# Performance work log

Hardware: AMD Instinct MI355X
Metric: run time of the kernel (lower is better)

## Reference

```python
import jax, jax.numpy as jnp
import numpy as np

NUM_USERS = 100000
NUM_ITEMS = 50000
N_NODES = NUM_USERS + NUM_ITEMS
N_INTERACTIONS = 1000000
LATENT_DIM = 32
K = 4
N_LAYERS = 3
BATCH = 4096


def setup_inputs() -> dict:
    key = jax.random.key(0)
    k_u, k_i = jax.random.split(key)
    # torch init: normal std=0.1
    user_emb = 0.1 * jax.random.normal(k_u, (NUM_USERS, LATENT_DIM * K), dtype=jnp.float32)
    item_emb = 0.1 * jax.random.normal(k_i, (NUM_ITEMS, LATENT_DIM * K), dtype=jnp.float32)
    # build symmetric normalized bipartite adjacency (LightGCN getSparseGraph)
    rng = np.random.default_rng(0)
    u = rng.integers(0, NUM_USERS, N_INTERACTIONS)
    it = rng.integers(0, NUM_ITEMS, N_INTERACTIONS)
    src = np.concatenate([u, it + NUM_USERS]).astype(np.int32)
    dst = np.concatenate([it + NUM_USERS, u]).astype(np.int32)
    deg = np.bincount(src, minlength=N_NODES).astype(np.float32)
    deg = np.maximum(deg, 1.0)
    val = (1.0 / np.sqrt(deg[src] * deg[dst])).astype(np.float32)
    users = rng.integers(0, NUM_USERS, BATCH).astype(np.int32)
    items = rng.integers(0, NUM_ITEMS, BATCH).astype(np.int32)
    return {
        "user_emb": user_emb,
        "item_emb": item_emb,
        "edge_src": jnp.asarray(src),
        "edge_dst": jnp.asarray(dst),
        "edge_val": jnp.asarray(val),
        "users": jnp.asarray(users),
        "items": jnp.asarray(items),
    }


def _computer(user_emb, item_emb, edge_src, edge_dst, edge_val):
    n_users = user_emb.shape[0]
    n = n_users + item_emb.shape[0]
    # [N, K, D] disentangled factor view of the K*D embedding
    x = jnp.concatenate([user_emb, item_emb], axis=0).reshape(n, K, -1)
    embs = [x]
    for _ in range(N_LAYERS):
        # SpMM over all K factor slices at once: out[dst] += val * x[src]
        msgs = x[edge_src] * edge_val[:, None, None]  # [E, K, D]
        x = jax.ops.segment_sum(msgs, edge_dst, num_segments=n)
        embs.append(x)
    light_out = jnp.mean(jnp.stack(embs, axis=1), axis=1)  # [N, K, D]
    return light_out[:n_users], light_out[n_users:]


def reference(user_emb, item_emb, edge_src, edge_dst, edge_val, users, items):
    all_users, all_items = _computer(user_emb, item_emb, edge_src, edge_dst, edge_val)
    u = all_users[users]   # [B, K, D]
    i = all_items[items]   # [B, K, D]
    return jnp.sum(u * i, axis=(-1, -2))  # [B]
```

## Files before the change

### kernel.cpp

```cpp
#include <hip/hip_runtime.h>

#define NUM_USERS 100000
#define NUM_ITEMS 50000
#define N_NODES   150000
#define N_EDGES   2000000
#define N_INTER   1000000
#define DIM       128
#define DIM4      32
#define BATCH     4096
#define B_SHIFT   9
#define BUCK_N    (1 << B_SHIFT)
#define NBUCK     ((N_NODES + BUCK_N - 1) >> B_SHIFT)
#define PAIRS     4096
#define NPBLK     ((N_INTER + PAIRS - 1) / PAIRS)
#define CAP       12288
#define CAPB      16384
#define MARK_BLOCKS 512
#define CONV_BLOCKS (((N_NODES + 1) * 8 + 255) / 256)

#define G0 16.0f
#define INV_G1 (1.0f / 64.0f)
#define INV_G2 (1.0f / 256.0f)

typedef __attribute__((ext_vector_type(4))) float f32x4;
typedef __attribute__((ext_vector_type(2))) float f32x2;

__device__ inline f32x2 f8x2_lo(unsigned w) { return __builtin_amdgcn_cvt_pk_f32_fp8(w, 0); }
__device__ inline f32x2 f8x2_hi(unsigned w) { return __builtin_amdgcn_cvt_pk_f32_fp8(w, 1); }
__device__ inline unsigned enc_lo(float a, float b, unsigned old) {
    return __builtin_amdgcn_cvt_pk_fp8_f32(a, b, old, 0);
}
__device__ inline unsigned enc_hi(float a, float b, unsigned old) {
    return __builtin_amdgcn_cvt_pk_fp8_f32(a, b, old, 1);
}


__global__ void bucket_scatter_kernel(const int* __restrict__ src,
                                      int* __restrict__ bcur,
                                      int* __restrict__ tmp) {
    __shared__ int lhist[NBUCK];
    __shared__ int lcur[NBUCK];
    int t = threadIdx.x;
    int base = blockIdx.x * PAIRS;
    for (int i = t; i < NBUCK; i += 512) lhist[i] = 0;
    __syncthreads();
    for (int i = 0; i < PAIRS / 512; ++i) {
        int gp = base + i * 512 + t;
        if (gp < N_INTER) {
            int u = src[gp];
            int v = src[N_INTER + gp];
            atomicAdd(&lhist[v >> B_SHIFT], 1);
            atomicAdd(&lhist[u >> B_SHIFT], 1);
        }
    }
    __syncthreads();
    for (int i = t; i < NBUCK; i += 512) {
        int c = lhist[i];
        lcur[i] = c ? (i * CAPB + atomicAdd(&bcur[i], c)) : 0;
    }
    __syncthreads();
    for (int i = 0; i < PAIRS / 512; ++i) {
        int gp = base + i * 512 + t;
        if (gp < N_INTER) {
            int u = src[gp];
            int v = src[N_INTER + gp];
            int bv = v >> B_SHIFT;
            int bu = u >> B_SHIFT;
            int pos0 = atomicAdd(&lcur[bv], 1);
            if (pos0 < (bv + 1) * CAPB)
                tmp[pos0] = (u << B_SHIFT) | (v & (BUCK_N - 1));
            int pos1 = atomicAdd(&lcur[bu], 1);
            if (pos1 < (bu + 1) * CAPB)
                tmp[pos1] = (v << B_SHIFT) | (u & (BUCK_N - 1));
        }
    }
}


__global__ void place_kernel(const int* __restrict__ bcur,
                             const int* __restrict__ tmp,
                             int* __restrict__ row_start,
                             float* __restrict__ rinv,
                             float* __restrict__ sdeg,
                             int* __restrict__ csr_src) {
    __shared__ int lhist[BUCK_N];
    __shared__ int lofs[BUCK_N];
    __shared__ int ssc[512];
    __shared__ int outbuf[CAP];
    int b = blockIdx.x;
    int t = threadIdx.x;

    int c = 0;
    if (t < NBUCK) {
        c = bcur[t];
        if (c > CAPB) c = CAPB;
    }
    ssc[t] = c;
    __syncthreads();
    for (int off = 1; off < 512; off <<= 1) {
        int v = (t >= off) ? ssc[t - off] : 0;
        __syncthreads();
        ssc[t] += v;
        __syncthreads();
    }
    int beg = (b == 0) ? 0 : ssc[b - 1];
    int end = ssc[b];
    int cnt = end - beg;
    int tbase = b * CAPB;
    int n0 = b << B_SHIFT;
    int n1 = n0 + BUCK_N; if (n1 > N_NODES) n1 = N_NODES;
    if (b == NBUCK - 1 && t == 0) row_start[N_NODES] = end;

    lhist[t] = 0;
    __syncthreads();
    for (int e = t; e < cnt; e += 512)
        atomicAdd(&lhist[tmp[tbase + e] & (BUCK_N - 1)], 1);
    __syncthreads();

    int v = lhist[t];
    ssc[t] = v;
    __syncthreads();
    for (int off = 1; off < 512; off <<= 1) {
        int u = (t >= off) ? ssc[t - off] : 0;
        __syncthreads();
        ssc[t] += u;
        __syncthreads();
    }
    int excl = ssc[t] - v;
    lofs[t] = excl;
    int node = n0 + t;
    if (node < n1) {
        row_start[node] = beg + excl;
        float d = (float)(v > 1 ? v : 1);
        float rr = rsqrtf(d);
        rinv[node] = rr;
        sdeg[node] = d * rr;
    }
    __syncthreads();

    if (cnt <= CAP) {
        for (int e = t; e < cnt; e += 512) {
            int p = tmp[tbase + e];
            int pos = atomicAdd(&lofs[p & (BUCK_N - 1)], 1);
            outbuf[pos] = p >> B_SHIFT;
        }
        __syncthreads();
        for (int i = t; i < cnt; i += 512) csr_src[beg + i] = outbuf[i];
    } else {
        for (int e = t; e < cnt; e += 512) {
            int p = tmp[tbase + e];
            int pos = atomicAdd(&lofs[p & (BUCK_N - 1)], 1);
            csr_src[beg + pos] = p >> B_SHIFT;
        }
    }
}


__global__ void mark_conv_kernel(const f32x4* __restrict__ ue4,
                                 const f32x4* __restrict__ ie4,
                                 const float* __restrict__ rinv,
                                 uint4* __restrict__ e16f8,
                                 uint4* __restrict__ w1f8,
                                 uint4* __restrict__ w2f8,
                                 const int* __restrict__ users,
                                 const int* __restrict__ items,
                                 const int* __restrict__ row_start,
                                 const int* __restrict__ csr_src,
                                 int* __restrict__ mark) {
    int bid = blockIdx.x;
    if (bid < MARK_BLOCKS) {
        int g = threadIdx.x >> 4;
        int lane = threadIdx.x & 15;
        int b = bid * 16 + g;
        int node = (b < BATCH) ? users[b] : (NUM_USERS + items[b - BATCH]);
        if (lane == 0) mark[node] = 1;
        int beg = row_start[node], end = row_start[node + 1];
        for (int e = beg + lane; e < end; e += 16) mark[csr_src[e]] = 1;
        return;
    }
    int i = (bid - MARK_BLOCKS) * 256 + threadIdx.x;
    const int total = (N_NODES + 1) * 8;
    if (i >= total) return;
    int n = i >> 3;
    if (n >= N_NODES) {
        uint4 z = make_uint4(0u, 0u, 0u, 0u);
        e16f8[i] = z;
        w1f8[i] = z;
        w2f8[i] = z;
        return;
    }
    int j = i & 7;
    const f32x4* row = (n < NUM_USERS) ? ue4 + (size_t)n * DIM4
                                       : ie4 + (size_t)(n - NUM_USERS) * DIM4;
    float r = rinv[n] * G0;
    f32x4 c0 = __builtin_nontemporal_load(&row[4 * j]);
    f32x4 c1 = __builtin_nontemporal_load(&row[4 * j + 1]);
    f32x4 c2 = __builtin_nontemporal_load(&row[4 * j + 2]);
    f32x4 c3 = __builtin_nontemporal_load(&row[4 * j + 3]);
    uint4 o;
    o.x = enc_hi(r * c0.z, r * c0.w, enc_lo(r * c0.x, r * c0.y, 0u));
    o.y = enc_hi(r * c1.z, r * c1.w, enc_lo(r * c1.x, r * c1.y, 0u));
    o.z = enc_hi(r * c2.z, r * c2.w, enc_lo(r * c2.x, r * c2.y, 0u));
    o.w = enc_hi(r * c3.z, r * c3.w, enc_lo(r * c3.x, r * c3.y, 0u));
    e16f8[i] = o;
}


__device__ inline void spmm_row(int n, const uint2* __restrict__ tabl,
                                const int* __restrict__ row_start,
                                const int* __restrict__ csr_src,
                                const float* __restrict__ rinv,
                                uint2* __restrict__ out,
                                int lane, int gbase) {
    int beg = row_start[n], end = row_start[n + 1];
    f32x2 a0 = {0.f, 0.f}, a1 = {0.f, 0.f}, a2 = {0.f, 0.f}, a3 = {0.f, 0.f};
    for (int base = beg; base < end; base += 16) {
        int eidx = base + lane;
        int myedge = (eidx < end) ? csr_src[eidx] : N_NODES;
        int s[16];
#pragma unroll
        for (int k = 0; k < 16; ++k) s[k] = __shfl(myedge, gbase + k, 64);
        uint2 h[16];
#pragma unroll
        for (int k = 0; k < 16; ++k) h[k] = tabl[s[k] << 4];
#pragma unroll
        for (int k = 0; k < 16; ++k) {
            a0 += f8x2_lo(h[k].x);
            a1 += f8x2_hi(h[k].x);
            a2 += f8x2_lo(h[k].y);
            a3 += f8x2_hi(h[k].y);
        }
    }
    float f = rinv[n];
    f = 4.0f * f * f;
    a0 *= f; a1 *= f; a2 *= f; a3 *= f;
    uint2 o;
    o.x = enc_hi(a1[0], a1[1], enc_lo(a0[0], a0[1], 0u));
    o.y = enc_hi(a3[0], a3[1], enc_lo(a2[0], a2[1], 0u));
    out[((size_t)n << 4) + lane] = o;
}

__global__ __launch_bounds__(256) void spmm_f8_kernel(
        const uint2* __restrict__ tab,
        const int* __restrict__ row_start,
        const int* __restrict__ csr_src,
        const float* __restrict__ rinv,
        uint2* __restrict__ out) {
    int t = threadIdx.x;
    int n = blockIdx.x * 16 + (t >> 4);
    if (n >= N_NODES) return;
    spmm_row(n, tab + (t & 15), row_start, csr_src, rinv, out, t & 15, t & 48);
}

__global__ __launch_bounds__(256) void spmm_f8_masked_kernel(
        const uint2* __restrict__ tab,
        const int* __restrict__ row_start,
        const int* __restrict__ csr_src,
        const float* __restrict__ rinv,
        const int* __restrict__ mark,
        uint2* __restrict__ out) {
    int t = threadIdx.x;
    int n = blockIdx.x * 16 + (t >> 4);
    if (n >= N_NODES) return;
    if (!mark[n]) return;
    spmm_row(n, tab + (t & 15), row_start, csr_src, rinv, out, t & 15, t & 48);
}


__global__ void epilogue_kernel(const f32x4* __restrict__ ue4,
                                const f32x4* __restrict__ ie4,
                                const uint2* __restrict__ w1f8,
                                const uint2* __restrict__ w2f8,
                                const int* __restrict__ row_start,
                                const int* __restrict__ csr_src,
                                const float* __restrict__ rinv,
                                const float* __restrict__ sdeg,
                                const int* __restrict__ users,
                                const int* __restrict__ items,
                                float* __restrict__ out) {
    int t = threadIdx.x;
    int elem = blockIdx.x * 4 + (t >> 5);
    int half = (t >> 4) & 1;
    int lane = t & 15;
    int gbase = t & 48;
    int node = half ? (NUM_USERS + items[elem]) : users[elem];

    const f32x4* erow = (node < NUM_USERS) ? ue4 + (size_t)node * DIM4
                                           : ie4 + (size_t)(node - NUM_USERS) * DIM4;
    f32x4 f0 = erow[2 * lane];
    f32x4 f1 = erow[2 * lane + 1];
    float a[8] = {f0.x, f0.y, f0.z, f0.w, f1.x, f1.y, f1.z, f1.w};

    float sd = sdeg[node];
    uint2 d1 = w1f8[(size_t)node * 16 + lane];
    uint2 d2 = w2f8[(size_t)node * 16 + lane];
    f32x2 p0 = f8x2_lo(d1.x), p1 = f8x2_hi(d1.x), p2 = f8x2_lo(d1.y), p3 = f8x2_hi(d1.y);
    f32x2 q0 = f8x2_lo(d2.x), q1 = f8x2_hi(d2.x), q2 = f8x2_lo(d2.y), q3 = f8x2_hi(d2.y);
    a[0] += sd * (p0[0] * INV_G1 + q0[0] * INV_G2);
    a[1] += sd * (p0[1] * INV_G1 + q0[1] * INV_G2);
    a[2] += sd * (p1[0] * INV_G1 + q1[0] * INV_G2);
    a[3] += sd * (p1[1] * INV_G1 + q1[1] * INV_G2);
    a[4] += sd * (p2[0] * INV_G1 + q2[0] * INV_G2);
    a[5] += sd * (p2[1] * INV_G1 + q2[1] * INV_G2);
    a[6] += sd * (p3[0] * INV_G1 + q3[0] * INV_G2);
    a[7] += sd * (p3[1] * INV_G1 + q3[1] * INV_G2);

    int beg = row_start[node], end = row_start[node + 1];
    f32x2 b0 = {0.f, 0.f}, b1 = {0.f, 0.f}, b2 = {0.f, 0.f}, b3 = {0.f, 0.f};
    const uint2* w2l = w2f8 + lane;
    for (int base = beg; base < end; base += 16) {
        int eidx = base + lane;
        int myedge = (eidx < end) ? csr_src[eidx] : N_NODES;
        int s[16];
#pragma unroll
        for (int k = 0; k < 16; ++k) s[k] = __shfl(myedge, gbase + k, 64);
        uint2 h[16];
#pragma unroll
        for (int k = 0; k < 16; ++k) h[k] = w2l[(size_t)s[k] << 4];
#pragma unroll
        for (int k = 0; k < 16; ++k) {
            b0 += f8x2_lo(h[k].x);
            b1 += f8x2_hi(h[k].x);
            b2 += f8x2_lo(h[k].y);
            b3 += f8x2_hi(h[k].y);
        }
    }
    float rv = rinv[node] * INV_G2;
    a[0] += rv * b0[0]; a[1] += rv * b0[1];
    a[2] += rv * b1[0]; a[3] += rv * b1[1];
    a[4] += rv * b2[0]; a[5] += rv * b2[1];
    a[6] += rv * b3[0]; a[7] += rv * b3[1];

    int wl = t & 63;
    float p = 0.f;
#pragma unroll
    for (int j = 0; j < 8; ++j) p += a[j] * __shfl(a[j], wl ^ 16, 64);
    for (int off = 8; off > 0; off >>= 1) p += __shfl_down(p, off, 16);
    if (half == 0 && lane == 0) out[elem] = p * (1.0f / 16.0f);
}

extern "C" void kernel_launch(void* const* d_in, const int* in_sizes, int n_in,
                              void* d_out, int out_size, void* d_ws, size_t ws_size,
                              hipStream_t stream) {
    const f32x4* ue4 = (const f32x4*)d_in[0];
    const f32x4* ie4 = (const f32x4*)d_in[1];
    const int*   src   = (const int*)d_in[2];
    const int*   users = (const int*)d_in[5];
    const int*   items = (const int*)d_in[6];
    float* out = (float*)d_out;

    const size_t frow = (size_t)(N_NODES + 1) * 16;
    char* ws = (char*)d_ws;
    uint2* e16f8 = (uint2*)ws;  ws += frow * sizeof(uint2);
    uint2* w1f8  = (uint2*)ws;  ws += frow * sizeof(uint2);
    uint2* w2f8  = (uint2*)ws;  ws += frow * sizeof(uint2);
    int*   row_start = (int*)ws;    ws += (size_t)(N_NODES + 1) * sizeof(int);
    float* rinv      = (float*)ws;  ws += (size_t)N_NODES * sizeof(float);
    float* sdeg      = (float*)ws;  ws += (size_t)N_NODES * sizeof(float);
    int*   mark      = (int*)ws;    ws += (size_t)N_NODES * sizeof(int);
    int*   bcur      = (int*)ws;    ws += (size_t)NBUCK * sizeof(int);
    ws = (char*)(((size_t)ws + 255) & ~(size_t)255);
    int*   tmp       = (int*)ws;    ws += (size_t)NBUCK * CAPB * sizeof(int);
    int*   csr_src   = (int*)ws;    ws += (size_t)N_EDGES * sizeof(int);

    hipMemsetAsync(mark, 0, (size_t)(N_NODES + NBUCK) * sizeof(int), stream);

    bucket_scatter_kernel<<<NPBLK, 512, 0, stream>>>(src, bcur, tmp);
    place_kernel<<<NBUCK, 512, 0, stream>>>(bcur, tmp, row_start, rinv, sdeg, csr_src);

    mark_conv_kernel<<<MARK_BLOCKS + CONV_BLOCKS, 256, 0, stream>>>(
        ue4, ie4, rinv, (uint4*)e16f8, (uint4*)w1f8, (uint4*)w2f8,
        users, items, row_start, csr_src, mark);

    spmm_f8_kernel<<<(N_NODES + 15) / 16, 256, 0, stream>>>(
        e16f8, row_start, csr_src, rinv, w1f8);

    spmm_f8_masked_kernel<<<(N_NODES + 15) / 16, 256, 0, stream>>>(
        w1f8, row_start, csr_src, rinv, mark, w2f8);

    epilogue_kernel<<<BATCH / 4, 128, 0, stream>>>(
        ue4, ie4, w1f8, w2f8, row_start, csr_src, rinv, sdeg, users, items, out);
}
```

Baseline: 247.7 us.

## Build CSR with a global degree histogram, three-pass scan and atomic fill

Replaces the two-kernel bucketed scatter and per-bucket local sort CSR build with a simpler pipeline. A global atomic degree count feeds a three-kernel prefix scan, then an atomic-cursor fill writes neighbours directly into csr_src. This drops the large tmp staging buffer and the shared-memory sorting, but adds more kernel launches and uncoalesced global atomics and scattered writes. Neighbour order within a row also becomes nondeterministic, which can change fp8 accumulation order in later layers.

```diff
diff --git a/kernel.cpp b/kernel.cpp
--- a/kernel.cpp
+++ b/kernel.cpp
@@ -8,13 +8,8 @@
 #define DIM       128
 #define DIM4      32
 #define BATCH     4096
-#define B_SHIFT   9
-#define BUCK_N    (1 << B_SHIFT)
-#define NBUCK     ((N_NODES + BUCK_N - 1) >> B_SHIFT)
-#define PAIRS     4096
-#define NPBLK     ((N_INTER + PAIRS - 1) / PAIRS)
-#define CAP       12288
-#define CAPB      16384
+#define SCAN_BLK  1024
+#define NSCAN     ((N_NODES + SCAN_BLK - 1) / SCAN_BLK)
 #define MARK_BLOCKS 512
 #define CONV_BLOCKS (((N_NODES + 1) * 8 + 255) / 256)
 
@@ -35,123 +30,88 @@
 }
 
 
-__global__ void bucket_scatter_kernel(const int* __restrict__ src,
-                                      int* __restrict__ bcur,
-                                      int* __restrict__ tmp) {
-    __shared__ int lhist[NBUCK];
-    __shared__ int lcur[NBUCK];
-    int t = threadIdx.x;
-    int base = blockIdx.x * PAIRS;
-    for (int i = t; i < NBUCK; i += 512) lhist[i] = 0;
+__global__ void deg_kernel(const int* __restrict__ src, int* __restrict__ deg) {
+    int i = blockIdx.x * 256 + threadIdx.x;
+    int stride = gridDim.x * 256;
+    for (; i < N_INTER; i += stride) {
+        int u = src[i];
+        int v = src[N_INTER + i];
+        atomicAdd(&deg[u], 1);
+        atomicAdd(&deg[v], 1);
+    }
+}
+
+__global__ __launch_bounds__(1024) void scanA_kernel(const int* __restrict__ deg,
+                                                     int* __restrict__ row_start,
+                                                     int* __restrict__ gsum,
+                                                     float* __restrict__ rinv,
+                                                     float* __restrict__ sdeg) {
+    __shared__ int wsum[16];
+    int b = blockIdx.x, t = threadIdx.x;
+    int i = b * SCAN_BLK + t;
+    int v = (i < N_NODES) ? deg[i] : 0;
+    int incl = v;
+#pragma unroll
+    for (int off = 1; off < 64; off <<= 1) {
+        int u = __shfl_up(incl, off, 64);
+        if ((t & 63) >= off) incl += u;
+    }
+    if ((t & 63) == 63) wsum[t >> 6] = incl;
     __syncthreads();
-    for (int i = 0; i < PAIRS / 512; ++i) {
-        int gp = base + i * 512 + t;
-        if (gp < N_INTER) {
-            int u = src[gp];
-            int v = src[N_INTER + gp];
-            atomicAdd(&lhist[v >> B_SHIFT], 1);
-            atomicAdd(&lhist[u >> B_SHIFT], 1);
-        }
-    }
-    __syncthreads();
-    for (int i = t; i < NBUCK; i += 512) {
-        int c = lhist[i];
-        lcur[i] = c ? (i * CAPB + atomicAdd(&bcur[i], c)) : 0;
-    }
-    __syncthreads();
-    for (int i = 0; i < PAIRS / 512; ++i) {
-        int gp = base + i * 512 + t;
-        if (gp < N_INTER) {
-            int u = src[gp];
-            int v = src[N_INTER + gp];
-            int bv = v >> B_SHIFT;
-            int bu = u >> B_SHIFT;
-            int pos0 = atomicAdd(&lcur[bv], 1);
-            if (pos0 < (bv + 1) * CAPB)
-                tmp[pos0] = (u << B_SHIFT) | (v & (BUCK_N - 1));
-            int pos1 = atomicAdd(&lcur[bu], 1);
-            if (pos1 < (bu + 1) * CAPB)
-                tmp[pos1] = (v << B_SHIFT) | (u & (BUCK_N - 1));
-        }
-    }
-}
-
-
-__global__ void place_kernel(const int* __restrict__ bcur,
-                             const int* __restrict__ tmp,
-                             int* __restrict__ row_start,
-                             float* __restrict__ rinv,
-                             float* __restrict__ sdeg,
-                             int* __restrict__ csr_src) {
-    __shared__ int lhist[BUCK_N];
-    __shared__ int lofs[BUCK_N];
-    __shared__ int ssc[512];
-    __shared__ int outbuf[CAP];
-    int b = blockIdx.x;
-    int t = threadIdx.x;
-
-    int c = 0;
-    if (t < NBUCK) {
-        c = bcur[t];
-        if (c > CAPB) c = CAPB;
-    }
-    ssc[t] = c;
-    __syncthreads();
-    for (int off = 1; off < 512; off <<= 1) {
-        int v = (t >= off) ? ssc[t - off] : 0;
-        __syncthreads();
-        ssc[t] += v;
-        __syncthreads();
-    }
-    int beg = (b == 0) ? 0 : ssc[b - 1];
-    int end = ssc[b];
-    int cnt = end - beg;
-    int tbase = b * CAPB;
-    int n0 = b << B_SHIFT;
-    int n1 = n0 + BUCK_N; if (n1 > N_NODES) n1 = N_NODES;
-    if (b == NBUCK - 1 && t == 0) row_start[N_NODES] = end;
-
-    lhist[t] = 0;
-    __syncthreads();
-    for (int e = t; e < cnt; e += 512)
-        atomicAdd(&lhist[tmp[tbase + e] & (BUCK_N - 1)], 1);
-    __syncthreads();
-
-    int v = lhist[t];
-    ssc[t] = v;
-    __syncthreads();
-    for (int off = 1; off < 512; off <<= 1) {
-        int u = (t >= off) ? ssc[t - off] : 0;
-        __syncthreads();
-        ssc[t] += u;
-        __syncthreads();
-    }
-    int excl = ssc[t] - v;
-    lofs[t] = excl;
-    int node = n0 + t;
-    if (node < n1) {
-        row_start[node] = beg + excl;
+    int add = 0;
+    int w = t >> 6;
+    for (int k = 0; k < w; ++k) add += wsum[k];
+    int excl = incl - v + add;
+    if (i < N_NODES) {
+        row_start[i] = excl;
         float d = (float)(v > 1 ? v : 1);
         float rr = rsqrtf(d);
-        rinv[node] = rr;
-        sdeg[node] = d * rr;
-    }
+        rinv[i] = rr;
+        sdeg[i] = d * rr;
+    }
+    if (t == SCAN_BLK - 1) gsum[b] = excl + v;
+}
+
+__global__ void scanB_kernel(const int* __restrict__ gsum,
+                             int* __restrict__ gofs,
+                             int* __restrict__ row_start) {
+    __shared__ int s[256];
+    int t = threadIdx.x;
+    int c = (t < NSCAN) ? gsum[t] : 0;
+    s[t] = c;
     __syncthreads();
-
-    if (cnt <= CAP) {
-        for (int e = t; e < cnt; e += 512) {
-            int p = tmp[tbase + e];
-            int pos = atomicAdd(&lofs[p & (BUCK_N - 1)], 1);
-            outbuf[pos] = p >> B_SHIFT;
-        }
+    for (int off = 1; off < 256; off <<= 1) {
+        int v = (t >= off) ? s[t - off] : 0;
         __syncthreads();
-        for (int i = t; i < cnt; i += 512) csr_src[beg + i] = outbuf[i];
-    } else {
-        for (int e = t; e < cnt; e += 512) {
-            int p = tmp[tbase + e];
-            int pos = atomicAdd(&lofs[p & (BUCK_N - 1)], 1);
-            csr_src[beg + pos] = p >> B_SHIFT;
-        }
+        s[t] += v;
+        __syncthreads();
+    }
+    if (t < NSCAN) gofs[t] = s[t] - c;
+    if (t == NSCAN - 1) row_start[N_NODES] = s[t];
+}
+
+__global__ __launch_bounds__(1024) void scanC_kernel(const int* __restrict__ gofs,
+                                                     int* __restrict__ row_start,
+                                                     int* __restrict__ cur) {
+    int b = blockIdx.x, t = threadIdx.x;
+    int i = b * SCAN_BLK + t;
+    if (i < N_NODES) {
+        int r = row_start[i] + gofs[b];
+        row_start[i] = r;
+        cur[i] = r;
+    }
+}
+
+__global__ void fill_kernel(const int* __restrict__ src,
+                            int* __restrict__ cur,
+                            int* __restrict__ csr_src) {
+    int i = blockIdx.x * 256 + threadIdx.x;
+    int stride = gridDim.x * 256;
+    for (; i < N_INTER; i += stride) {
+        int u = src[i];
+        int v = src[N_INTER + i];
+        csr_src[atomicAdd(&cur[v], 1)] = u;
+        csr_src[atomicAdd(&cur[u], 1)] = v;
     }
 }
 
@@ -358,15 +318,20 @@
     float* rinv      = (float*)ws;  ws += (size_t)N_NODES * sizeof(float);
     float* sdeg      = (float*)ws;  ws += (size_t)N_NODES * sizeof(float);
     int*   mark      = (int*)ws;    ws += (size_t)N_NODES * sizeof(int);
-    int*   bcur      = (int*)ws;    ws += (size_t)NBUCK * sizeof(int);
+    int*   deg       = (int*)ws;    ws += (size_t)N_NODES * sizeof(int);
+    int*   cur       = (int*)ws;    ws += (size_t)N_NODES * sizeof(int);
+    int*   gsum      = (int*)ws;    ws += (size_t)NSCAN * sizeof(int);
+    int*   gofs      = (int*)ws;    ws += (size_t)NSCAN * sizeof(int);
     ws = (char*)(((size_t)ws + 255) & ~(size_t)255);
-    int*   tmp       = (int*)ws;    ws += (size_t)NBUCK * CAPB * sizeof(int);
     int*   csr_src   = (int*)ws;    ws += (size_t)N_EDGES * sizeof(int);
 
-    hipMemsetAsync(mark, 0, (size_t)(N_NODES + NBUCK) * sizeof(int), stream);
-
-    bucket_scatter_kernel<<<NPBLK, 512, 0, stream>>>(src, bcur, tmp);
-    place_kernel<<<NBUCK, 512, 0, stream>>>(bcur, tmp, row_start, rinv, sdeg, csr_src);
+    hipMemsetAsync(mark, 0, (size_t)(2 * N_NODES) * sizeof(int), stream);
+
+    deg_kernel<<<2048, 256, 0, stream>>>(src, deg);
+    scanA_kernel<<<NSCAN, SCAN_BLK, 0, stream>>>(deg, row_start, gsum, rinv, sdeg);
+    scanB_kernel<<<1, 256, 0, stream>>>(gsum, gofs, row_start);
+    scanC_kernel<<<NSCAN, SCAN_BLK, 0, stream>>>(gofs, row_start, cur);
+    fill_kernel<<<2048, 256, 0, stream>>>(src, cur, csr_src);
 
     mark_conv_kernel<<<MARK_BLOCKS + CONV_BLOCKS, 256, 0, stream>>>(
         ue4, ie4, rinv, (uint4*)e16f8, (uint4*)w1f8, (uint4*)w2f8,
```

New measurement: 463.7 us. +87.2%, slower.
